# Optimization experiments

Measured on AMD Instinct MI355X. Metric: run time of the kernel, lower is better.

## Reference

```python
import jax, jax.numpy as jnp
import numpy as np

V = 9488  # vocab_size + 1
H = 512   # rnn_size = att_hid_size = input_encoding_size
F = 2048  # fc/att feat size

def setup_inputs() -> dict:
    key = jax.random.key(0)
    ks = jax.random.split(key, 16)
    s = 0.02
    return {
        'fc_feats': jax.random.normal(ks[0], (64, F), jnp.float32),
        'att_feats': jax.random.normal(ks[1], (64, 196, F), jnp.float32),
        'seq': jax.random.randint(ks[2], (64, 17), 0, 9487),
        'lin_W': jax.random.normal(ks[3], (H, F), jnp.float32) * s,
        'lin_b': jnp.zeros((H,), jnp.float32),
        'emb': jax.random.uniform(ks[4], (V, H), jnp.float32, -0.1, 0.1),
        'Wih': jax.random.normal(ks[5], (4 * H, H + F), jnp.float32) * s,
        'Whh': jax.random.normal(ks[6], (4 * H, H), jnp.float32) * s,
        'ctx_W': jax.random.normal(ks[7], (H, F), jnp.float32) * s,
        'ctx_b': jnp.zeros((H,), jnp.float32),
        'h2a_W': jax.random.normal(ks[8], (H, H), jnp.float32) * s,
        'h2a_b': jnp.zeros((H,), jnp.float32),
        'alpha_W': jax.random.normal(ks[9], (1, H), jnp.float32) * s,
        'alpha_b': jnp.zeros((1,), jnp.float32),
        'logit_W': jax.random.uniform(ks[10], (V, H), jnp.float32, -0.1, 0.1),
        'logit_b': jnp.zeros((V,), jnp.float32),
    }

def reference(fc_feats, att_feats, seq, lin_W, lin_b, emb, Wih, Whh,
              ctx_W, ctx_b, h2a_W, h2a_b, alpha_W, alpha_b, logit_W, logit_b):
    # init_hidden: h0 = c0 = Linear(fc_feats)  -> [B, H]
    h0 = fc_feats @ lin_W.T + lin_b
    # ctx2att(att_feats) is constant across timesteps -> compute once. [B, L, H]
    p_att = jnp.einsum('blf,hf->blh', att_feats, ctx_W) + ctx_b
    tokens = seq[:, :-1].T  # [T-1, B]

    def step(carry, it):
        h, c = carry
        xt = emb[it]                                   # [B, H]
        att_h = h @ h2a_W.T + h2a_b                    # [B, H]
        dot = jnp.tanh(p_att + att_h[:, None, :])      # [B, L, H]
        e = jnp.einsum('blh,h->bl', dot, alpha_W[0]) + alpha_b[0]
        w = jax.nn.softmax(e, axis=-1)                 # [B, L]
        att_res = jnp.einsum('bl,blf->bf', w, att_feats)  # [B, F]
        x = jnp.concatenate([xt, att_res], axis=1)     # [B, H+F]
        gates = x @ Wih.T + h @ Whh.T                  # bias=False LSTM
        i_g, f_g, g_g, o_g = jnp.split(gates, 4, axis=1)  # torch order i,f,g,o
        c_n = jax.nn.sigmoid(f_g) * c + jax.nn.sigmoid(i_g) * jnp.tanh(g_g)
        h_n = jax.nn.sigmoid(o_g) * jnp.tanh(c_n)
        logp = jax.nn.log_softmax(h_n @ logit_W.T + logit_b, axis=-1)
        return (h_n, c_n), logp

    _, outs = jax.lax.scan(step, (h0, h0), tokens)     # [T-1, B, V]
    return jnp.transpose(outs, (1, 0, 2))              # [B, T-1, V]
```

## Files before the change

### kernel.cpp

```cpp
#include <hip/hip_runtime.h>
#include <stdint.h>
#include <stddef.h>

#define BB 64
#define LL 196
#define FF 2048
#define HH 512
#define VV 9488
#define NPAD 9600
#define TT 16
#define KXX 3072
#define MM (BB * LL)

typedef short short8 __attribute__((ext_vector_type(8)));
typedef short short4v __attribute__((ext_vector_type(4)));
typedef float f32x4 __attribute__((ext_vector_type(4)));
typedef unsigned short u16;

typedef __attribute__((address_space(3))) uint32_t lds_u32_t;
typedef __attribute__((address_space(1))) const uint32_t glb_u32_t;

__device__ __forceinline__ u16 f2bf(float f) {
  uint32_t u = __builtin_bit_cast(uint32_t, f);
  u += 0x7FFFu + ((u >> 16) & 1u);
  return (u16)(u >> 16);
}
__device__ __forceinline__ float bf2f(u16 s) {
  return __builtin_bit_cast(float, ((uint32_t)s) << 16);
}
__device__ __forceinline__ float fast_tanh(float x) {
  return 1.0f - 2.0f / (1.0f + __expf(2.0f * x));
}
__device__ __forceinline__ float fast_sig(float x) {
  return 1.0f / (1.0f + __expf(-x));
}
__device__ __forceinline__ float wred_sum(float v) {
#pragma unroll
  for (int o = 32; o; o >>= 1) v += __shfl_xor(v, o, 64);
  return v;
}
__device__ __forceinline__ float wred_max(float v) {
#pragma unroll
  for (int o = 32; o; o >>= 1) v = fmaxf(v, __shfl_xor(v, o, 64));
  return v;
}
__device__ __forceinline__ f32x4 mfma16(short8 a, short8 b, f32x4 c) {
  return __builtin_amdgcn_mfma_f32_16x16x32_bf16(a, b, c, 0, 0, 0);
}
__device__ __forceinline__ short8 ldbf(const u16* p) {
  return *reinterpret_cast<const short8*>(p);
}
__device__ __forceinline__ void gload16(const u16* g, u16* l) {
  __builtin_amdgcn_global_load_lds((glb_u32_t*)g, (lds_u32_t*)l, 16, 0, 0);
}

__global__ __launch_bounds__(256) void k_setup(
    const float* __restrict__ ctx_W, u16* __restrict__ ctxWb,
    const float* __restrict__ lin_W, u16* __restrict__ linWb,
    const float* __restrict__ h2a_W, u16* __restrict__ h2aWb,
    const float* __restrict__ logit_W, u16* __restrict__ lWb,
    const float* __restrict__ fc, u16* __restrict__ fcb,
    const float* __restrict__ attf, u16* __restrict__ attb,
    const float* __restrict__ Wih, const float* __restrict__ Whh, u16* __restrict__ Wc,
    const float* __restrict__ emb, const int* __restrict__ seq, u16* __restrict__ Xemb) {
  int blk = blockIdx.x, t = threadIdx.x;
  if (blk < 32264) {
    const float* s; u16* d; int rel;
    if (blk < 1024)      { s = ctx_W;   d = ctxWb; rel = blk; }
    else if (blk < 2048) { s = lin_W;   d = linWb; rel = blk - 1024; }
    else if (blk < 2304) { s = h2a_W;   d = h2aWb; rel = blk - 2048; }
    else if (blk < 7048) { s = logit_W; d = lWb;   rel = blk - 2304; }
    else if (blk < 7176) { s = fc;      d = fcb;   rel = blk - 7048; }
    else                 { s = attf;    d = attb;  rel = blk - 7176; }
    int i = rel * 256 + t;
    float4 v = reinterpret_cast<const float4*>(s)[i];
    ushort4 o; o.x = f2bf(v.x); o.y = f2bf(v.y); o.z = f2bf(v.z); o.w = f2bf(v.w);
    reinterpret_cast<ushort4*>(d)[i] = o;
  } else if (blk < 38408) {
    int i = (blk - 32264) * 256 + t;
    int idx = i * 4;
    int n = idx / KXX, k = idx - n * KXX;
    const float* p = (k < 2560) ? (Wih + (size_t)n * 2560 + k) : (Whh + (size_t)n * HH + (k - 2560));
    float4 v = *reinterpret_cast<const float4*>(p);
    ushort4 o; o.x = f2bf(v.x); o.y = f2bf(v.y); o.z = f2bf(v.z); o.w = f2bf(v.w);
    reinterpret_cast<ushort4*>(Wc)[i] = o;
  } else {
    int i = (blk - 38408) * 256 + t;
    int idx = i * 4;
    int tt = idx / (BB * HH);
    int r = idx - tt * (BB * HH);
    int b = r / HH, k = r - b * HH;
    int tok = seq[b * 17 + tt];
    float4 v = *reinterpret_cast<const float4*>(emb + (size_t)tok * HH + k);
    ushort4 o; o.x = f2bf(v.x); o.y = f2bf(v.y); o.z = f2bf(v.z); o.w = f2bf(v.w);
    reinterpret_cast<ushort4*>(Xemb)[i] = o;
  }
}

__global__ __launch_bounds__(256) void k_h0(const u16* __restrict__ fcb, const u16* __restrict__ linWb,
                                            const float* __restrict__ lin_b,
                                            u16* __restrict__ hb, float* __restrict__ c) {
  int lane = threadIdx.x & 63;
  int m0 = (threadIdx.x >> 6) * 16, n0 = blockIdx.x * 16;
  const u16* xr = fcb + (size_t)(m0 + (lane & 15)) * FF + ((lane >> 4) * 8);
  const u16* wr = linWb + (size_t)(n0 + (lane & 15)) * FF + ((lane >> 4) * 8);
  f32x4 acc = {0.f, 0.f, 0.f, 0.f};
#pragma unroll 8
  for (int kk = 0; kk < 64; ++kk)
    acc = mfma16(ldbf(xr + kk * 32), ldbf(wr + kk * 32), acc);
  int col = n0 + (lane & 15);
  float bias = lin_b[col];
#pragma unroll
  for (int j = 0; j < 4; ++j) {
    int row = m0 + (lane >> 4) * 4 + j;
    float v = acc[j] + bias;
    hb[row * HH + col] = f2bf(v);
    c[row * HH + col] = v;
  }
}

__global__ __launch_bounds__(512) void k_patt(const u16* __restrict__ attb,
                                              const u16* __restrict__ ctxWb, const float* __restrict__ ctx_b,
                                              u16* __restrict__ p_att) {
  __shared__ __align__(16) u16 As[128][32];
  __shared__ __align__(16) u16 Bs[128][32];
  int d = blockIdx.x;
  int bid = (d & 7) * 49 + (d >> 3);
  int mb = bid >> 2, nb = bid & 3;
  int m0 = mb * 128, n0 = nb * 128;
  int tid = threadIdx.x;
  int wid = tid >> 6, lane = tid & 63;
  int wr2 = wid >> 2, wc2 = wid & 3;
  int ar = lane & 15, ak = (lane >> 4) * 8;
  const u16* ga = attb + (size_t)(m0 + (tid >> 2)) * FF + (tid & 3) * 8;
  const u16* gb = ctxWb + (size_t)(n0 + (tid >> 2)) * FF + (tid & 3) * 8;
  u16* la = &As[0][0] + tid * 8;
  u16* lb = &Bs[0][0] + tid * 8;

  f32x4 zero = {0.f, 0.f, 0.f, 0.f};
  f32x4 acc[4][2];
#pragma unroll
  for (int i = 0; i < 4; ++i)
#pragma unroll
    for (int j = 0; j < 2; ++j) acc[i][j] = zero;

  for (int ks = 0; ks < 64; ++ks) {
    int k0 = ks * 32;
    __syncthreads();
    gload16(ga + k0, la);
    gload16(gb + k0, lb);
    __syncthreads();
    short8 af[4], bfr[2];
#pragma unroll
    for (int i = 0; i < 4; ++i)
      af[i] = *reinterpret_cast<const short8*>(&As[wr2 * 64 + i * 16 + ar][ak]);
#pragma unroll
    for (int j = 0; j < 2; ++j)
      bfr[j] = *reinterpret_cast<const short8*>(&Bs[wc2 * 32 + j * 16 + ar][ak]);
#pragma unroll
    for (int i = 0; i < 4; ++i)
#pragma unroll
      for (int j = 0; j < 2; ++j)
        acc[i][j] = mfma16(af[i], bfr[j], acc[i][j]);
  }
#pragma unroll
  for (int j = 0; j < 2; ++j) {
    int col = n0 + wc2 * 32 + j * 16 + ar;
    float bias = ctx_b[col];
#pragma unroll
    for (int i = 0; i < 4; ++i)
#pragma unroll
      for (int q = 0; q < 4; ++q) {
        int row = m0 + wr2 * 64 + i * 16 + (lane >> 4) * 4 + q;
        p_att[(size_t)row * HH + col] = f2bf(acc[i][j][q] + bias);
      }
  }
}

__device__ __forceinline__ void dev_atth(int nt, const u16* __restrict__ hb, const u16* __restrict__ h2aWb,
                                         const float* __restrict__ h2ab, float* __restrict__ ah) {
  int lane = threadIdx.x & 63;
  int m0 = (threadIdx.x >> 6) * 16, n0 = nt * 16;
  int ak = (lane >> 4) * 8;
  const u16* xr = hb + (size_t)(m0 + (lane & 15)) * HH + ak;
  const u16* wr = h2aWb + (size_t)(n0 + (lane & 15)) * HH + ak;
  f32x4 acc = {0.f, 0.f, 0.f, 0.f};
#pragma unroll
  for (int kk = 0; kk < 16; ++kk)
    acc = mfma16(ldbf(xr + kk * 32), ldbf(wr + kk * 32), acc);
  int col = n0 + (lane & 15);
  float bias = h2ab[col];
#pragma unroll
  for (int j = 0; j < 4; ++j)
    ah[(size_t)(m0 + (lane >> 4) * 4 + j) * HH + col] = acc[j] + bias;
}

__device__ __forceinline__ void dev_e(int bid4, const u16* __restrict__ p_att, const float* __restrict__ ah,
                                      const float* __restrict__ alphaW, const float* __restrict__ alphab,
                                      float* __restrict__ e) {
  int gw = bid4 * 4 + (threadIdx.x >> 6);
  int lane = threadIdx.x & 63;
  int b = gw / LL, l = gw - b * LL;
  short8 pa = ldbf(p_att + (size_t)gw * HH + lane * 8);
  const float4* ap = reinterpret_cast<const float4*>(ah + (size_t)b * HH + lane * 8);
  float4 a0 = ap[0], a1 = ap[1];
  const float4* wp = reinterpret_cast<const float4*>(alphaW + lane * 8);
  float4 w0 = wp[0], w1 = wp[1];
  float s = fast_tanh(bf2f((u16)pa[0]) + a0.x) * w0.x
          + fast_tanh(bf2f((u16)pa[1]) + a0.y) * w0.y
          + fast_tanh(bf2f((u16)pa[2]) + a0.z) * w0.z
          + fast_tanh(bf2f((u16)pa[3]) + a0.w) * w0.w
          + fast_tanh(bf2f((u16)pa[4]) + a1.x) * w1.x
          + fast_tanh(bf2f((u16)pa[5]) + a1.y) * w1.y
          + fast_tanh(bf2f((u16)pa[6]) + a1.z) * w1.z
          + fast_tanh(bf2f((u16)pa[7]) + a1.w) * w1.w;
  s = wred_sum(s);
  if (!lane) e[b * 256 + l] = s + alphab[0];
}

__global__ __launch_bounds__(256) void k_atth(const u16* __restrict__ hb, const u16* __restrict__ h2aWb,
                                              const float* __restrict__ h2ab, float* __restrict__ ah) {
  dev_atth(blockIdx.x, hb, h2aWb, h2ab, ah);
}
__global__ __launch_bounds__(256) void k_e(const u16* __restrict__ p_att, const float* __restrict__ ah,
                                           const float* __restrict__ alphaW, const float* __restrict__ alphab,
                                           float* __restrict__ e) {
  dev_e(blockIdx.x, p_att, ah, alphaW, alphab, e);
}

__global__ __launch_bounds__(256) void k_attR(const float* __restrict__ e, const u16* __restrict__ attb,
                                              u16* __restrict__ xatt) {
  __shared__ float w_s[LL];
  __shared__ float red[8];
  __shared__ float part[4][256];
  int b = blockIdx.x >> 3, f8 = blockIdx.x & 7;
  int t = threadIdx.x, wid = t >> 6, lane = t & 63;
  float ev = (t < LL) ? e[b * 256 + t] : -1e30f;
  float m = wred_max(ev);
  if (!lane) red[wid] = m;
  __syncthreads();
  m = fmaxf(fmaxf(red[0], red[1]), fmaxf(red[2], red[3]));
  float ex = __expf(ev - m);
  float s = wred_sum(ex);
  if (!lane) red[4 + wid] = s;
  __syncthreads();
  s = red[4] + red[5] + red[6] + red[7];
  if (t < LL) w_s[t] = ex / s;
  __syncthreads();

  int f0 = f8 * 256 + lane * 4;
  float a0 = 0.f, a1 = 0.f, a2 = 0.f, a3 = 0.f;
  int l0 = wid * 49;
  const u16* ap = attb + ((size_t)(b * LL + l0)) * FF + f0;
#pragma unroll 7
  for (int l = 0; l < 49; ++l) {
    float wv = w_s[l0 + l];
    short4v av = *reinterpret_cast<const short4v*>(ap);
    ap += FF;
    a0 += wv * bf2f((u16)av[0]); a1 += wv * bf2f((u16)av[1]);
    a2 += wv * bf2f((u16)av[2]); a3 += wv * bf2f((u16)av[3]);
  }
  *reinterpret_cast<float4*>(&part[wid][lane * 4]) = make_float4(a0, a1, a2, a3);
  __syncthreads();
  float v = part[0][t] + part[1][t] + part[2][t] + part[3][t];
  xatt[(size_t)b * FF + f8 * 256 + t] = f2bf(v);
}

__global__ __launch_bounds__(256) void k_gatelstm(const u16* __restrict__ Xemb, const u16* __restrict__ xatt,
                                                  const u16* __restrict__ hb_in, const u16* __restrict__ Wc,
                                                  float* __restrict__ c, u16* __restrict__ hb_out, int tstep) {
  __shared__ float sm[4][4][16][16];
  int jt = blockIdx.x >> 2, mq = blockIdx.x & 3;
  int m0 = mq * 16;
  int lane = threadIdx.x & 63, kq = threadIdx.x >> 6;
  int ar = lane & 15, ak8 = (lane >> 4) * 8;
  int m = m0 + ar;
  int wn = jt * 16 + ar;
  f32x4 zero = {0.f, 0.f, 0.f, 0.f};
  f32x4 acc[4] = {zero, zero, zero, zero};
  const u16* xr0 = Xemb + ((size_t)tstep * BB + m) * HH;
  const u16* xr1 = xatt + (size_t)m * FF;
  const u16* xr2 = hb_in + (size_t)m * HH;

#pragma unroll 4
  for (int kk = 0; kk < 24; ++kk) {
    int k = kq * 768 + kk * 32 + ak8;
    short8 a;
    if (k < 512)       a = ldbf(xr0 + k);
    else if (k < 2560) a = ldbf(xr1 + (k - 512));
    else               a = ldbf(xr2 + (k - 2560));
    short8 bv[4];
#pragma unroll
    for (int g = 0; g < 4; ++g)
      bv[g] = ldbf(Wc + (size_t)(g * 512 + wn) * KXX + k);
#pragma unroll
    for (int g = 0; g < 4; ++g) acc[g] = mfma16(a, bv[g], acc[g]);
  }
#pragma unroll
  for (int g = 0; g < 4; ++g)
#pragma unroll
    for (int q = 0; q < 4; ++q)
      sm[kq][g][(lane >> 4) * 4 + q][ar] = acc[g][q];
  __syncthreads();
  int r = threadIdx.x >> 4, cc = threadIdx.x & 15;
  float gi = sm[0][0][r][cc] + sm[1][0][r][cc] + sm[2][0][r][cc] + sm[3][0][r][cc];
  float gf = sm[0][1][r][cc] + sm[1][1][r][cc] + sm[2][1][r][cc] + sm[3][1][r][cc];
  float gg = sm[0][2][r][cc] + sm[1][2][r][cc] + sm[2][2][r][cc] + sm[3][2][r][cc];
  float go = sm[0][3][r][cc] + sm[1][3][r][cc] + sm[2][3][r][cc] + sm[3][3][r][cc];
  int idx = (m0 + r) * HH + jt * 16 + cc;
  float cn = fast_sig(gf) * c[idx] + fast_sig(gi) * fast_tanh(gg);
  float hn = fast_sig(go) * fast_tanh(cn);
  c[idx] = cn;
  hb_out[idx] = f2bf(hn);
}

__global__ __launch_bounds__(256) void k_logall(const u16* __restrict__ XhL, const u16* __restrict__ lWb,
                                                const float* __restrict__ lb, float* __restrict__ out) {
  __shared__ __align__(16) u16 As[128][32];
  __shared__ __align__(16) u16 Bs[128][32];
  int d = blockIdx.x;
  int mb = d & 7, nb = d >> 3;
  int m0 = mb * 128, n0 = nb * 128;
  int tid = threadIdx.x;
  int wid = tid >> 6, lane = tid & 63;
  int wr = wid >> 1, wc = wid & 1;
  int ar = lane & 15, ak = (lane >> 4) * 8;
  int rt = tid >> 1, st = tid & 1;
  const u16* agp = XhL + (size_t)(m0 + rt) * HH + st * 16;
  const u16* bgp = lWb + (size_t)(n0 + rt) * HH + st * 16;

  f32x4 zero = {0.f, 0.f, 0.f, 0.f};
  f32x4 acc[4][4];
#pragma unroll
  for (int i = 0; i < 4; ++i)
#pragma unroll
    for (int j = 0; j < 4; ++j) acc[i][j] = zero;

  for (int ks = 0; ks < 16; ++ks) {
    int k0 = ks * 32;
    short8 a0 = ldbf(agp + k0);
    short8 a1 = ldbf(agp + k0 + 8);
    short8 b0 = ldbf(bgp + k0);
    short8 b1 = ldbf(bgp + k0 + 8);
    __syncthreads();
    *reinterpret_cast<short8*>(&As[rt][st * 16]) = a0;
    *reinterpret_cast<short8*>(&As[rt][st * 16 + 8]) = a1;
    *reinterpret_cast<short8*>(&Bs[rt][st * 16]) = b0;
    *reinterpret_cast<short8*>(&Bs[rt][st * 16 + 8]) = b1;
    __syncthreads();
    short8 af[4], bfr[4];
#pragma unroll
    for (int i = 0; i < 4; ++i)
      af[i] = *reinterpret_cast<const short8*>(&As[wr * 64 + i * 16 + ar][ak]);
#pragma unroll
    for (int j = 0; j < 4; ++j)
      bfr[j] = *reinterpret_cast<const short8*>(&Bs[wc * 64 + j * 16 + ar][ak]);
#pragma unroll
    for (int i = 0; i < 4; ++i)
#pragma unroll
      for (int j = 0; j < 4; ++j)
        acc[i][j] = mfma16(af[i], bfr[j], acc[i][j]);
  }
#pragma unroll
  for (int j = 0; j < 4; ++j) {
    int col = n0 + wc * 64 + j * 16 + ar;
    if (col >= VV) continue;
    float bias = lb[col];
#pragma unroll
    for (int i = 0; i < 4; ++i)
#pragma unroll
      for (int q = 0; q < 4; ++q) {
        int row = m0 + wr * 64 + i * 16 + (lane >> 4) * 4 + q;
        int bb = row & 63, ts = row >> 6;
        out[((size_t)(bb * TT + ts)) * VV + col] = acc[i][j][q] + bias;
      }
  }
}

__global__ __launch_bounds__(256) void k_lsmall(float* __restrict__ out) {
  __shared__ float red[8];
  float* row = out + (size_t)blockIdx.x * VV;
  float4* row4 = reinterpret_cast<float4*>(row);
  int t = threadIdx.x, wid = t >> 6, lane = t & 63;
  float4 v[10];
  float m = -1e30f;
#pragma unroll
  for (int p = 0; p < 10; ++p) {
    int i4 = p * 256 + t;
    if (i4 < VV / 4) {
      v[p] = row4[i4];
      m = fmaxf(m, fmaxf(fmaxf(v[p].x, v[p].y), fmaxf(v[p].z, v[p].w)));
    } else {
      v[p] = make_float4(-1e30f, -1e30f, -1e30f, -1e30f);
    }
  }
  m = wred_max(m);
  if (!lane) red[wid] = m;
  __syncthreads();
  m = fmaxf(fmaxf(red[0], red[1]), fmaxf(red[2], red[3]));
  float s = 0.f;
#pragma unroll
  for (int p = 0; p < 10; ++p)
    s += __expf(v[p].x - m) + __expf(v[p].y - m) + __expf(v[p].z - m) + __expf(v[p].w - m);
  s = wred_sum(s);
  if (!lane) red[4 + wid] = s;
  __syncthreads();
  s = red[4] + red[5] + red[6] + red[7];
  float lse = m + __logf(s);
#pragma unroll
  for (int p = 0; p < 10; ++p) {
    int i4 = p * 256 + t;
    if (i4 < VV / 4)
      row4[i4] = make_float4(v[p].x - lse, v[p].y - lse, v[p].z - lse, v[p].w - lse);
  }
}

extern "C" void kernel_launch(void* const* d_in, const int* in_sizes, int n_in,
                              void* d_out, int out_size, void* d_ws, size_t ws_size,
                              hipStream_t stream) {
  const float* fc      = (const float*)d_in[0];
  const float* attf    = (const float*)d_in[1];
  const int*   seq     = (const int*)d_in[2];
  const float* lin_W   = (const float*)d_in[3];
  const float* lin_b   = (const float*)d_in[4];
  const float* emb     = (const float*)d_in[5];
  const float* Wih     = (const float*)d_in[6];
  const float* Whh     = (const float*)d_in[7];
  const float* ctx_W   = (const float*)d_in[8];
  const float* ctx_b   = (const float*)d_in[9];
  const float* h2a_W   = (const float*)d_in[10];
  const float* h2a_b   = (const float*)d_in[11];
  const float* alpha_W = (const float*)d_in[12];
  const float* alpha_b = (const float*)d_in[13];
  const float* logit_W = (const float*)d_in[14];
  const float* logit_b = (const float*)d_in[15];
  float* out = (float*)d_out;

  char* base = (char*)d_ws;
  size_t off = 0;
  auto alloc = [&](size_t bytes) -> char* {
    off = (off + 255) & ~(size_t)255;
    char* p = base + off;
    off += bytes;
    return p;
  };
  u16*   p_att  = (u16*)alloc((size_t)MM * HH * 2);
  u16*   ctxWb  = (u16*)alloc((size_t)HH * FF * 2);
  u16*   linWb  = (u16*)alloc((size_t)HH * FF * 2);
  u16*   fcb    = (u16*)alloc((size_t)BB * FF * 2);
  u16*   h2aWb  = (u16*)alloc((size_t)HH * HH * 2);
  u16*   Xemb   = (u16*)alloc((size_t)TT * BB * HH * 2);
  float* c      = (float*)alloc((size_t)BB * HH * 4);
  u16*   Xh     = (u16*)alloc((size_t)(TT + 1) * BB * HH * 2);
  u16*   xatt   = (u16*)alloc((size_t)BB * FF * 2);
  float* eb     = (float*)alloc((size_t)BB * 256 * 4);
  float* ah     = (float*)alloc((size_t)BB * HH * 4);
  u16*   Wc     = (u16*)alloc((size_t)2048 * KXX * 2);
  u16*   lWb    = (u16*)alloc((size_t)NPAD * HH * 2);
  u16*   attb   = (u16*)alloc((size_t)MM * FF * 2);
  (void)ws_size;

  k_setup<<<38920, 256, 0, stream>>>(ctx_W, ctxWb, lin_W, linWb, h2a_W, h2aWb, logit_W, lWb,
                                     fc, fcb, attf, attb, Wih, Whh, Wc, emb, seq, Xemb);
  k_h0<<<32, 256, 0, stream>>>(fcb, linWb, lin_b, Xh, c);
  k_patt<<<392, 512, 0, stream>>>(attb, ctxWb, ctx_b, p_att);

  k_atth<<<32, 256, 0, stream>>>(Xh, h2aWb, h2a_b, ah);
  k_e<<<MM / 4, 256, 0, stream>>>(p_att, ah, alpha_W, alpha_b, eb);

  for (int t = 0; t < TT; ++t) {
    u16* ht  = Xh + (size_t)t * BB * HH;
    u16* htn = Xh + (size_t)(t + 1) * BB * HH;
    k_attR<<<512, 256, 0, stream>>>(eb, attb, xatt);
    k_gatelstm<<<128, 256, 0, stream>>>(Xemb, xatt, ht, Wc, c, htn, t);
    if (t < TT - 1) {
      k_atth<<<32, 256, 0, stream>>>(htn, h2aWb, h2a_b, ah);
      k_e<<<MM / 4, 256, 0, stream>>>(p_att, ah, alpha_W, alpha_b, eb);
    }
  }
  k_logall<<<600, 256, 0, stream>>>(Xh + (size_t)BB * HH, lWb, logit_b, out);
  k_lsmall<<<TT * BB, 256, 0, stream>>>(out);
}
```

Before: 788.3 us.

## Use FP8 copy of attention features in per-step weighted sum, fuse h0 into patt

Setup also writes an FP8 (e4m3) copy of att_feats when workspace allows, and the per-timestep attention-weighted reduction reads that copy instead of bf16, halving its memory traffic across all 16 steps. The h0 linear is folded into the p_att GEMM launch as extra blocks, removing one kernel launch. The gate/LSTM kernel block index is swizzled across groups of eight. FP8 loses precision in att_res, and setup writes an extra 25 MB buffer.

Result: faster. 705.8 us (-10.5%).

```diff
diff --git a/kernel.cpp b/kernel.cpp
--- a/kernel.cpp
+++ b/kernel.cpp
@@ -16,6 +16,7 @@
 typedef short short4v __attribute__((ext_vector_type(4)));
 typedef float f32x4 __attribute__((ext_vector_type(4)));
 typedef unsigned short u16;
+typedef unsigned char u8;
 
 typedef __attribute__((address_space(3))) uint32_t lds_u32_t;
 typedef __attribute__((address_space(1))) const uint32_t glb_u32_t;
@@ -60,22 +61,28 @@
     const float* __restrict__ h2a_W, u16* __restrict__ h2aWb,
     const float* __restrict__ logit_W, u16* __restrict__ lWb,
     const float* __restrict__ fc, u16* __restrict__ fcb,
-    const float* __restrict__ attf, u16* __restrict__ attb,
+    const float* __restrict__ attf, u16* __restrict__ attb, u8* __restrict__ att8,
     const float* __restrict__ Wih, const float* __restrict__ Whh, u16* __restrict__ Wc,
     const float* __restrict__ emb, const int* __restrict__ seq, u16* __restrict__ Xemb) {
   int blk = blockIdx.x, t = threadIdx.x;
   if (blk < 32264) {
     const float* s; u16* d; int rel;
+    bool isAtt = false;
     if (blk < 1024)      { s = ctx_W;   d = ctxWb; rel = blk; }
     else if (blk < 2048) { s = lin_W;   d = linWb; rel = blk - 1024; }
     else if (blk < 2304) { s = h2a_W;   d = h2aWb; rel = blk - 2048; }
     else if (blk < 7048) { s = logit_W; d = lWb;   rel = blk - 2304; }
     else if (blk < 7176) { s = fc;      d = fcb;   rel = blk - 7048; }
-    else                 { s = attf;    d = attb;  rel = blk - 7176; }
+    else                 { s = attf;    d = attb;  rel = blk - 7176; isAtt = true; }
     int i = rel * 256 + t;
     float4 v = reinterpret_cast<const float4*>(s)[i];
     ushort4 o; o.x = f2bf(v.x); o.y = f2bf(v.y); o.z = f2bf(v.z); o.w = f2bf(v.w);
     reinterpret_cast<ushort4*>(d)[i] = o;
+    if (isAtt && att8) {
+      uint32_t p8 = __builtin_amdgcn_cvt_pk_fp8_f32(v.x, v.y, 0u, false);
+      p8 = __builtin_amdgcn_cvt_pk_fp8_f32(v.z, v.w, p8, true);
+      reinterpret_cast<uint32_t*>(att8)[i] = p8;
+    }
   } else if (blk < 38408) {
     int i = (blk - 32264) * 256 + t;
     int idx = i * 4;
@@ -97,11 +104,11 @@
   }
 }
 
-__global__ __launch_bounds__(256) void k_h0(const u16* __restrict__ fcb, const u16* __restrict__ linWb,
-                                            const float* __restrict__ lin_b,
-                                            u16* __restrict__ hb, float* __restrict__ c) {
+__device__ __forceinline__ void dev_h0(int nt, const u16* __restrict__ fcb, const u16* __restrict__ linWb,
+                                       const float* __restrict__ lin_b,
+                                       u16* __restrict__ hb, float* __restrict__ c) {
   int lane = threadIdx.x & 63;
-  int m0 = (threadIdx.x >> 6) * 16, n0 = blockIdx.x * 16;
+  int m0 = (threadIdx.x >> 6) * 16, n0 = nt * 16;
   const u16* xr = fcb + (size_t)(m0 + (lane & 15)) * FF + ((lane >> 4) * 8);
   const u16* wr = linWb + (size_t)(n0 + (lane & 15)) * FF + ((lane >> 4) * 8);
   f32x4 acc = {0.f, 0.f, 0.f, 0.f};
@@ -121,10 +128,17 @@
 
 __global__ __launch_bounds__(512) void k_patt(const u16* __restrict__ attb,
                                               const u16* __restrict__ ctxWb, const float* __restrict__ ctx_b,
-                                              u16* __restrict__ p_att) {
+                                              u16* __restrict__ p_att,
+                                              const u16* __restrict__ fcb, const u16* __restrict__ linWb,
+                                              const float* __restrict__ lin_b,
+                                              u16* __restrict__ hb0, float* __restrict__ c) {
   __shared__ __align__(16) u16 As[128][32];
   __shared__ __align__(16) u16 Bs[128][32];
   int d = blockIdx.x;
+  if (d >= 392) {
+    if (threadIdx.x < 256) dev_h0(d - 392, fcb, linWb, lin_b, hb0, c);
+    return;
+  }
   int bid = (d & 7) * 49 + (d >> 3);
   int mb = bid >> 2, nb = bid & 3;
   int m0 = mb * 128, n0 = nb * 128;
@@ -228,8 +242,9 @@
   dev_e(blockIdx.x, p_att, ah, alphaW, alphab, e);
 }
 
+template<bool FP8>
 __global__ __launch_bounds__(256) void k_attR(const float* __restrict__ e, const u16* __restrict__ attb,
-                                              u16* __restrict__ xatt) {
+                                              const u8* __restrict__ att8, u16* __restrict__ xatt) {
   __shared__ float w_s[LL];
   __shared__ float red[8];
   __shared__ float part[4][256];
@@ -251,14 +266,28 @@
   int f0 = f8 * 256 + lane * 4;
   float a0 = 0.f, a1 = 0.f, a2 = 0.f, a3 = 0.f;
   int l0 = wid * 49;
-  const u16* ap = attb + ((size_t)(b * LL + l0)) * FF + f0;
+  if (FP8) {
+    const u8* ap = att8 + ((size_t)(b * LL + l0)) * FF + f0;
 #pragma unroll 7
-  for (int l = 0; l < 49; ++l) {
-    float wv = w_s[l0 + l];
-    short4v av = *reinterpret_cast<const short4v*>(ap);
-    ap += FF;
-    a0 += wv * bf2f((u16)av[0]); a1 += wv * bf2f((u16)av[1]);
-    a2 += wv * bf2f((u16)av[2]); a3 += wv * bf2f((u16)av[3]);
+    for (int l = 0; l < 49; ++l) {
+      float wv = w_s[l0 + l];
+      uint32_t pv = *reinterpret_cast<const uint32_t*>(ap);
+      ap += FF;
+      a0 += wv * __builtin_amdgcn_cvt_f32_fp8(pv, 0);
+      a1 += wv * __builtin_amdgcn_cvt_f32_fp8(pv, 1);
+      a2 += wv * __builtin_amdgcn_cvt_f32_fp8(pv, 2);
+      a3 += wv * __builtin_amdgcn_cvt_f32_fp8(pv, 3);
+    }
+  } else {
+    const u16* ap = attb + ((size_t)(b * LL + l0)) * FF + f0;
+#pragma unroll 7
+    for (int l = 0; l < 49; ++l) {
+      float wv = w_s[l0 + l];
+      short4v av = *reinterpret_cast<const short4v*>(ap);
+      ap += FF;
+      a0 += wv * bf2f((u16)av[0]); a1 += wv * bf2f((u16)av[1]);
+      a2 += wv * bf2f((u16)av[2]); a3 += wv * bf2f((u16)av[3]);
+    }
   }
   *reinterpret_cast<float4*>(&part[wid][lane * 4]) = make_float4(a0, a1, a2, a3);
   __syncthreads();
@@ -270,7 +299,9 @@
                                                   const u16* __restrict__ hb_in, const u16* __restrict__ Wc,
                                                   float* __restrict__ c, u16* __restrict__ hb_out, int tstep) {
   __shared__ float sm[4][4][16][16];
-  int jt = blockIdx.x >> 2, mq = blockIdx.x & 3;
+  int d = blockIdx.x;
+  int bid = (d & 7) * 16 + (d >> 3);
+  int jt = bid >> 2, mq = bid & 3;
   int m0 = mq * 16;
   int lane = threadIdx.x & 63, kq = threadIdx.x >> 6;
   int ar = lane & 15, ak8 = (lane >> 4) * 8;
@@ -458,12 +489,12 @@
   u16*   Wc     = (u16*)alloc((size_t)2048 * KXX * 2);
   u16*   lWb    = (u16*)alloc((size_t)NPAD * HH * 2);
   u16*   attb   = (u16*)alloc((size_t)MM * FF * 2);
-  (void)ws_size;
+  bool useF8 = (((off + 255) & ~(size_t)255) + (size_t)MM * FF) <= ws_size;
+  u8* att8 = useF8 ? (u8*)alloc((size_t)MM * FF) : nullptr;
 
   k_setup<<<38920, 256, 0, stream>>>(ctx_W, ctxWb, lin_W, linWb, h2a_W, h2aWb, logit_W, lWb,
-                                     fc, fcb, attf, attb, Wih, Whh, Wc, emb, seq, Xemb);
-  k_h0<<<32, 256, 0, stream>>>(fcb, linWb, lin_b, Xh, c);
-  k_patt<<<392, 512, 0, stream>>>(attb, ctxWb, ctx_b, p_att);
+                                     fc, fcb, attf, attb, att8, Wih, Whh, Wc, emb, seq, Xemb);
+  k_patt<<<424, 512, 0, stream>>>(attb, ctxWb, ctx_b, p_att, fcb, linWb, lin_b, Xh, c);
 
   k_atth<<<32, 256, 0, stream>>>(Xh, h2aWb, h2a_b, ah);
   k_e<<<MM / 4, 256, 0, stream>>>(p_att, ah, alpha_W, alpha_b, eb);
@@ -471,7 +502,8 @@
   for (int t = 0; t < TT; ++t) {
     u16* ht  = Xh + (size_t)t * BB * HH;
     u16* htn = Xh + (size_t)(t + 1) * BB * HH;
-    k_attR<<<512, 256, 0, stream>>>(eb, attb, xatt);
+    if (useF8) k_attR<true><<<512, 256, 0, stream>>>(eb, attb, att8, xatt);
+    else       k_attR<false><<<512, 256, 0, stream>>>(eb, attb, att8, xatt);
     k_gatelstm<<<128, 256, 0, stream>>>(Xemb, xatt, ht, Wc, c, htn, t);
     if (t < TT - 1) {
       k_atth<<<32, 256, 0, stream>>>(htn, h2aWb, h2a_b, ah);
```
